# Kernel optimization log

Hardware: AMD Instinct MI355X
Metric: run time of the kernel (lower is better)

The kernel has to match this reference:

```python
import jax, jax.numpy as jnp
import numpy as np

H_DIM = 2048
D_FF = 4 * H_DIM
NUM_EXPERTS = 8
NUM_SHARED = 2
BATCH, SEQ = 2, 2048


def setup_inputs() -> dict:
    key = jax.random.key(0)
    ks = jax.random.split(key, 10)
    s = 0.02
    return {
        "x": jax.random.normal(ks[0], (BATCH, SEQ, H_DIM), dtype=jnp.float32),
        "ws_w1": jax.random.normal(ks[1], (NUM_SHARED, H_DIM, D_FF), dtype=jnp.float32) * s,
        "ws_b1": jnp.zeros((NUM_SHARED, D_FF), dtype=jnp.float32),
        "ws_w2": jax.random.normal(ks[2], (NUM_SHARED, D_FF, H_DIM), dtype=jnp.float32) * s,
        "ws_b2": jnp.zeros((NUM_SHARED, H_DIM), dtype=jnp.float32),
        "we_w1": jax.random.normal(ks[3], (NUM_EXPERTS, H_DIM, D_FF), dtype=jnp.float32) * s,
        "we_b1": jnp.zeros((NUM_EXPERTS, D_FF), dtype=jnp.float32),
        "we_w2": jax.random.normal(ks[4], (NUM_EXPERTS, D_FF, H_DIM), dtype=jnp.float32) * s,
        "we_b2": jnp.zeros((NUM_EXPERTS, H_DIM), dtype=jnp.float32),
        "wg": jax.random.normal(ks[5], (H_DIM, NUM_EXPERTS), dtype=jnp.float32) * s,
        "top_k": 2,
    }


def reference(x, ws_w1, ws_b1, ws_w2, ws_b2, we_w1, we_b1, we_w2, we_b2, wg, top_k):
    B, S, D = x.shape
    xt = x.reshape(-1, D)  # [T, D], T = B*S
    T = xt.shape[0]

    # ---- shared experts: sum over NUM_SHARED dense MLPs ----
    hs = jax.nn.relu(jnp.einsum('td,ndf->ntf', xt, ws_w1) + ws_b1[:, None, :])
    shared = jnp.einsum('ntf,nfd->td', hs, ws_w2) + ws_b2.sum(axis=0)  # [T, D]

    # ---- sparse top-k routed MoE ----
    logits = xt @ wg                       # [T, E] router logits
    probs = jax.nn.softmax(logits, axis=-1)
    topv, topi = jax.lax.top_k(probs, top_k)
    gates = jnp.zeros_like(probs).at[jnp.arange(T)[:, None], topi].set(topv)  # [T, E]

    moe = jnp.zeros_like(xt)
    for e in range(we_w1.shape[0]):  # small fixed expert count
        he = jax.nn.relu(xt @ we_w1[e] + we_b1[e])
        ye = he @ we_w2[e] + we_b2[e]
        moe = moe + gates[:, e:e + 1] * ye

    out = (shared + moe).reshape(B, S, D)
    return out, logits
```

## Files before the change

kernel.cpp:

```cpp
#include <hip/hip_runtime.h>

#define TOKENS 4096
#define HD 2048
#define FF 8192
#define NE 8
#define NS 2
#define YHALF 33554432

typedef __attribute__((ext_vector_type(8))) short bf16x8;
typedef __attribute__((ext_vector_type(4))) float f32x4;

__device__ __forceinline__ unsigned rnd_bf(unsigned u) {
  return u + 0x7fffu + ((u >> 16) & 1u);
}
__device__ __forceinline__ unsigned short f2bf(float f) {
  unsigned u = __builtin_bit_cast(unsigned, f);
  return (unsigned short)(rnd_bf(u) >> 16);
}

#define GLDS16(gp, lp)                                                         \
  __builtin_amdgcn_global_load_lds(                                            \
      (const __attribute__((address_space(1))) unsigned*)(const void*)(gp),    \
      (__attribute__((address_space(3))) unsigned*)(lp), 16, 0, 0)

__global__ void cast_x_kernel(const float* __restrict__ x, unsigned short* __restrict__ xb) {
  const size_t i = ((size_t)blockIdx.x * 256 + threadIdx.x) * 4;
  float4 v = *(const float4*)(x + i);
  ushort4 o;
  o.x = f2bf(v.x); o.y = f2bf(v.y); o.z = f2bf(v.z); o.w = f2bf(v.w);
  *(ushort4*)(xb + i) = o;
}

__global__ void router_kernel(const float* __restrict__ x, const float* __restrict__ wg,
                              float* __restrict__ logits_out, int* __restrict__ topi,
                              float* __restrict__ topv, int* __restrict__ counts) {
  const int wave = threadIdx.x >> 6, lane = threadIdx.x & 63;
  const int t = blockIdx.x * 4 + wave;
  const float* xr = x + (size_t)t * HD;
  float acc[8];
#pragma unroll
  for (int e = 0; e < 8; ++e) acc[e] = 0.f;
  for (int d = lane; d < HD; d += 64) {
    const float xv = xr[d];
    const float4 w0 = *(const float4*)(wg + (size_t)d * 8);
    const float4 w1 = *(const float4*)(wg + (size_t)d * 8 + 4);
    acc[0] += xv * w0.x; acc[1] += xv * w0.y; acc[2] += xv * w0.z; acc[3] += xv * w0.w;
    acc[4] += xv * w1.x; acc[5] += xv * w1.y; acc[6] += xv * w1.z; acc[7] += xv * w1.w;
  }
#pragma unroll
  for (int e = 0; e < 8; ++e) {
#pragma unroll
    for (int off = 32; off > 0; off >>= 1) acc[e] += __shfl_xor(acc[e], off);
  }
  if (lane == 0) {
    *(float4*)(logits_out + (size_t)t * 8)     = make_float4(acc[0], acc[1], acc[2], acc[3]);
    *(float4*)(logits_out + (size_t)t * 8 + 4) = make_float4(acc[4], acc[5], acc[6], acc[7]);
    float mx = acc[0];
#pragma unroll
    for (int e = 1; e < 8; ++e) mx = fmaxf(mx, acc[e]);
    float p[8], s = 0.f;
#pragma unroll
    for (int e = 0; e < 8; ++e) { p[e] = expf(acc[e] - mx); s += p[e]; }
    const float inv = 1.f / s;
    int i1 = 0;
#pragma unroll
    for (int e = 1; e < 8; ++e) if (acc[e] > acc[i1]) i1 = e;
    int i2 = (i1 == 0) ? 1 : 0;
#pragma unroll
    for (int e = 0; e < 8; ++e) if (e != i1 && acc[e] > acc[i2]) i2 = e;
    topi[2 * t]     = i1; topv[2 * t]     = p[i1] * inv;
    topi[2 * t + 1] = i2; topv[2 * t + 1] = p[i2] * inv;
    atomicAdd(&counts[i1], 1);
    atomicAdd(&counts[i2], 1);
  }
}

__global__ void offs_kernel(const int* __restrict__ counts, int* __restrict__ offs,
                            int* __restrict__ cursors) {
  if (threadIdx.x == 0) {
    int r = 0;
    for (int e = 0; e < NE; ++e) { offs[e] = r; cursors[e] = r; r += counts[e]; }
  }
}

__global__ void gather_kernel(const unsigned short* __restrict__ xb,
                              const int* __restrict__ topi, const float* __restrict__ topv,
                              int* __restrict__ cursors, unsigned short* __restrict__ xg,
                              int* __restrict__ row_token, float* __restrict__ row_gate,
                              int* __restrict__ row_of) {
  const int wave = threadIdx.x >> 6, lane = threadIdx.x & 63;
  const int t = blockIdx.x * 4 + wave;
  const uint4* src = (const uint4*)(xb + (size_t)t * HD);
#pragma unroll
  for (int j = 0; j < 2; ++j) {
    const int e = topi[2 * t + j];
    int pos = 0;
    if (lane == 0) {
      pos = atomicAdd(&cursors[e], 1);
      row_token[pos] = t;
      row_gate[pos] = topv[2 * t + j];
      row_of[2 * t + j] = pos;
    }
    pos = __shfl(pos, 0);
    uint4* dst = (uint4*)(xg + (size_t)pos * HD);
#pragma unroll
    for (int c = lane; c < 256; c += 64) dst[c] = src[c];
  }
}

template <int K, int N>
__global__ __launch_bounds__(256) void pack_wt(const float* __restrict__ we,
                                               const float* __restrict__ ws,
                                               unsigned short* __restrict__ dstw) {
  const int e = blockIdx.z;
  const float* src = (e < NE) ? (we + (size_t)e * K * N) : (ws + (size_t)(e - NE) * K * N);
  unsigned short* dst = dstw + (size_t)e * K * N;
  const int nt = blockIdx.x * 64;
  const int kt = blockIdx.y * 64;
  __shared__ unsigned short t[64][73];
  const int tid = threadIdx.x;
  const int rr = tid >> 4, cc = (tid & 15) * 4;
#pragma unroll
  for (int i = 0; i < 4; ++i) {
    const int k = rr + i * 16;
    float4 v = *(const float4*)(src + (size_t)(kt + k) * N + nt + cc);
    t[k][cc + 0] = f2bf(v.x);
    t[k][cc + 1] = f2bf(v.y);
    t[k][cc + 2] = f2bf(v.z);
    t[k][cc + 3] = f2bf(v.w);
  }
  __syncthreads();
  const int nr = tid >> 2, kc = (tid & 3) * 16;
  unsigned u[8];
#pragma unroll
  for (int j = 0; j < 8; ++j)
    u[j] = (unsigned)t[kc + 2 * j][nr] | ((unsigned)t[kc + 2 * j + 1][nr] << 16);
  unsigned short* dp = dst + (size_t)(nt + nr) * K + kt + kc;
  uint4 v0; v0.x = u[0]; v0.y = u[1]; v0.z = u[2]; v0.w = u[3];
  uint4 v1; v1.x = u[4]; v1.y = u[5]; v1.z = u[6]; v1.w = u[7];
  *(uint4*)dp = v0;
  *(uint4*)(dp + 8) = v1;
}

template <int MS>
__device__ __forceinline__ void rd_a(bf16x8 (&d)[8], const unsigned short* base,
                                     int wr, int fr, int fq, int swz) {
#pragma unroll
  for (int mi = 0; mi < 4; ++mi)
#pragma unroll
    for (int ks = 0; ks < 2; ++ks)
      d[mi * 2 + ks] = *(const bf16x8*)(base + (wr * 128 + MS * 64 + mi * 16 + fr) * 64 +
                                        (((ks * 4 + fq) ^ swz) << 3));
}
template <int NSUB>
__device__ __forceinline__ void rd_b(bf16x8 (&d)[4], const unsigned short* base,
                                     int wc, int fr, int fq, int swz) {
#pragma unroll
  for (int ni = 0; ni < 2; ++ni)
#pragma unroll
    for (int ks = 0; ks < 2; ++ks)
      d[ni * 2 + ks] = *(const bf16x8*)(base + (wc * 64 + NSUB * 32 + ni * 16 + fr) * 64 +
                                        (((ks * 4 + fq) ^ swz) << 3));
}
template <int MS, int NSUB>
__device__ __forceinline__ void mm16(f32x4 (&acc)[8][4], const bf16x8 (&a)[8],
                                     const bf16x8 (&b)[4]) {
  __builtin_amdgcn_s_setprio(1);
#pragma unroll
  for (int mi = 0; mi < 4; ++mi)
#pragma unroll
    for (int ni = 0; ni < 2; ++ni)
#pragma unroll
      for (int ks = 0; ks < 2; ++ks)
        acc[MS * 4 + mi][NSUB * 2 + ni] = __builtin_amdgcn_mfma_f32_16x16x32_bf16(
            a[mi * 2 + ks], b[ni * 2 + ks], acc[MS * 4 + mi][NSUB * 2 + ni], 0, 0, 0);
  __builtin_amdgcn_s_setprio(0);
}

template <int K>
__device__ __forceinline__ void kloop(
    const unsigned short* __restrict__ A, const unsigned short* __restrict__ Bt,
    unsigned short* smem, int m0, int n0, f32x4 (&acc)[8][4],
    int wr, int wc, int fr, int fq, int swz,
    int wrA, int wcB, int lr8, int lc8, int scol, int kt0, int nkt) {
#define SAK(s, kt, b)                                                          \
  { const int r0_ = wrA + (s) * 64 + lr8;                                      \
    const unsigned short* s_ = A + (size_t)(m0 + r0_) * K + (kt) * 64 + scol;  \
    unsigned short* d_ = smem + (b) * 32768 + r0_ * 64 + lc8 * 8;              \
    GLDS16(s_, d_); GLDS16(s_ + (size_t)8 * K, d_ + 8 * 64); }
#define SBK(s, kt, b)                                                          \
  { const int r0_ = wcB + (s) * 32 + lr8;                                      \
    const unsigned short* s_ = Bt + (size_t)(n0 + r0_) * K + (kt) * 64 + scol; \
    unsigned short* d_ = smem + (b) * 32768 + 16384 + r0_ * 64 + lc8 * 8;      \
    GLDS16(s_, d_); GLDS16(s_ + (size_t)8 * K, d_ + 8 * 64); }

  SAK(0, kt0, 0); SAK(1, kt0, 0); SBK(0, kt0, 0); SBK(1, kt0, 0);
  SAK(0, kt0 + 1, 1); SAK(1, kt0 + 1, 1); SBK(0, kt0 + 1, 1); SBK(1, kt0 + 1, 1);
  asm volatile("s_waitcnt vmcnt(8)" ::: "memory");
  __builtin_amdgcn_s_barrier();

  bf16x8 a0[8], a1[8], b0[4], b1[4];
  rd_a<0>(a0, smem, wr, fr, fq, swz);
  rd_b<0>(b0, smem + 16384, wc, fr, fq, swz);

  for (int t = 0; t < nkt; ++t) {
    const int cur = t & 1;
    const int tp2 = kt0 + ((t + 2 < nkt) ? t + 2 : t);
    const unsigned short* As_c = smem + cur * 32768;
    const unsigned short* Bs_c = As_c + 16384;
    const unsigned short* As_n = smem + (cur ^ 1) * 32768;
    const unsigned short* Bs_n = As_n + 16384;
    rd_b<1>(b1, Bs_c, wc, fr, fq, swz);
    mm16<0, 0>(acc, a0, b0);
    rd_a<1>(a1, As_c, wr, fr, fq, swz);
    mm16<0, 1>(acc, a0, b1);
    asm volatile("s_waitcnt lgkmcnt(0)" ::: "memory");
    __builtin_amdgcn_s_barrier();
    __builtin_amdgcn_sched_barrier(0);
    SAK(0, tp2, cur); SBK(0, tp2, cur);
    mm16<1, 0>(acc, a1, b0);
    asm volatile("s_waitcnt vmcnt(4)" ::: "memory");
    __builtin_amdgcn_s_barrier();
    __builtin_amdgcn_sched_barrier(0);
    rd_a<0>(a0, As_n, wr, fr, fq, swz);
    rd_b<0>(b0, Bs_n, wc, fr, fq, swz);
    SAK(1, tp2, cur); SBK(1, tp2, cur);
    mm16<1, 1>(acc, a1, b1);
  }
#undef SAK
#undef SBK
}

__global__ __launch_bounds__(512, 2) void g1k(
    const unsigned short* __restrict__ Ash, const unsigned short* __restrict__ Art,
    const unsigned short* __restrict__ wt1,
    const float* __restrict__ bE, const float* __restrict__ bS,
    unsigned short* __restrict__ hout,
    const int* __restrict__ counts, const int* __restrict__ offs,
    int do_pack, const float* __restrict__ we_w2, const float* __restrict__ ws_w2,
    unsigned short* __restrict__ wt2) {
  constexpr int K = HD;
  constexpr int NBX = FF / 256;
  constexpr int NWG = NBX * 16;
  extern __shared__ unsigned short smem[];

  const int e = blockIdx.z;
  int M;
  const unsigned short* A;
  const float* bias;
  int hbase;
  if (e < NE) {
    M = counts[e];
    A = Art + (size_t)offs[e] * K;
    bias = bE + (size_t)e * FF;
    hbase = offs[e];
  } else {
    M = TOKENS;
    A = Ash;
    bias = bS + (size_t)(e - NE) * FF;
    hbase = 2 * TOKENS + (e - NE) * TOKENS;
  }
  const unsigned short* Bt = wt1 + (size_t)e * HD * FF;

  int flat = blockIdx.x + NBX * blockIdx.y;
  flat = (flat & 7) * (NWG >> 3) + (flat >> 3);
  const int m0 = (flat & 15) * 256;
  const int n0 = (flat >> 4) * 256;
  const int tid = threadIdx.x;

  if (m0 >= M) {
    if (!do_pack) return;
    int total = 0, prefix = 0;
    for (int e2 = 0; e2 < NE; ++e2) {
      int mb = (counts[e2] + 255) >> 8; if (mb > 16) mb = 16;
      const int inv = 32 * (16 - mb);
      if (e2 < e) prefix += inv;
      total += inv;
    }
    int mb_e = (counts[e] + 255) >> 8; if (mb_e > 16) mb_e = 16;
    const int m_idx = flat & 15, n_idx = flat >> 4;
    const int rank = prefix + n_idx * (16 - mb_e) + (m_idx - mb_e);
    unsigned short* ps = smem;
    const int NT = 10 * 128 * 32;
    const int kk = tid >> 3, cc = (tid & 7) * 8;
    float4 r0a, r0b;
    int i = rank;
    if (i < NT) {
      const int e2 = i >> 12, rem = i & 4095, ktt = rem >> 5, ntt = rem & 31;
      const float* src = (e2 < NE) ? (we_w2 + (size_t)e2 * FF * HD)
                                   : (ws_w2 + (size_t)(e2 - NE) * FF * HD);
      const float* sp = src + (size_t)(ktt * 64 + kk) * HD + ntt * 64 + cc;
      r0a = *(const float4*)sp; r0b = *(const float4*)(sp + 4);
    }
    int it = 0;
    while (i < NT) {
      const int inext = i + total;
      float4 r1a, r1b;
      if (inext < NT) {
        const int e2 = inext >> 12, rem = inext & 4095, ktt = rem >> 5, ntt = rem & 31;
        const float* src = (e2 < NE) ? (we_w2 + (size_t)e2 * FF * HD)
                                     : (ws_w2 + (size_t)(e2 - NE) * FF * HD);
        const float* sp = src + (size_t)(ktt * 64 + kk) * HD + ntt * 64 + cc;
        r1a = *(const float4*)sp; r1b = *(const float4*)(sp + 4);
      }
      unsigned short* pb = ps + (it & 1) * (64 * 73);
      {
        unsigned short* tp = pb + kk * 73 + cc;
        tp[0] = f2bf(r0a.x); tp[1] = f2bf(r0a.y); tp[2] = f2bf(r0a.z); tp[3] = f2bf(r0a.w);
        tp[4] = f2bf(r0b.x); tp[5] = f2bf(r0b.y); tp[6] = f2bf(r0b.z); tp[7] = f2bf(r0b.w);
      }
      __syncthreads();
      {
        const int e2 = i >> 12, rem = i & 4095, ktt = rem >> 5, ntt = rem & 31;
        unsigned short* dst = wt2 + (size_t)e2 * HD * FF;
        const int nn = tid >> 3, kc = (tid & 7) * 8;
        unsigned u[4];
#pragma unroll
        for (int j = 0; j < 4; ++j)
          u[j] = (unsigned)pb[(kc + 2 * j) * 73 + nn] |
                 ((unsigned)pb[(kc + 2 * j + 1) * 73 + nn] << 16);
        uint4 v; v.x = u[0]; v.y = u[1]; v.z = u[2]; v.w = u[3];
        *(uint4*)(dst + (size_t)(ntt * 64 + nn) * FF + ktt * 64 + kc) = v;
      }
      r0a = r1a; r0b = r1b;
      i = inext; ++it;
    }
    return;
  }

  const int wid = tid >> 6, ln = tid & 63;
  const int wr = wid >> 2, wc = wid & 3;
  const int fr = ln & 15, fq = ln >> 4;
  const int swz = fr & 7;
  const int lr8 = ln >> 3;
  const int lc8 = ln & 7;
  const int scol = (lc8 ^ lr8) << 3;
  const int wrA = wr * 128 + wc * 16;
  const int wcB = wc * 64 + wr * 16;

  f32x4 acc[8][4];
#pragma unroll
  for (int i = 0; i < 8; ++i)
#pragma unroll
    for (int j = 0; j < 4; ++j) acc[i][j] = (f32x4){0.f, 0.f, 0.f, 0.f};

  kloop<K>(A, Bt, smem, m0, n0, acc, wr, wc, fr, fq, swz, wrA, wcB, lr8, lc8, scol,
           0, K / 64);

#pragma unroll
  for (int nn = 0; nn < 4; ++nn) {
#pragma unroll
    for (int mm = 0; mm < 8; ++mm) {
      const int col = n0 + wc * 64 + (nn >> 1) * 32 + (nn & 1) * 16 + fr;
      const float bb = bias[col];
#pragma unroll
      for (int j = 0; j < 4; ++j) {
        const int r = m0 + wr * 128 + (mm >> 2) * 64 + (mm & 3) * 16 + fq * 4 + j;
        if (r < M) {
          float v = acc[mm][nn][j] + bb;
          v = v > 0.f ? v : 0.f;
          hout[(size_t)(hbase + r) * FF + col] = f2bf(v);
        }
      }
    }
  }
}

__global__ __launch_bounds__(512, 2) void g2k(
    const unsigned short* __restrict__ hbuf, const unsigned short* __restrict__ wt2,
    const float* __restrict__ bE, const float* __restrict__ bS,
    float* __restrict__ ybuf,
    const int* __restrict__ counts, const int* __restrict__ offs) {
  constexpr int K = FF;
  constexpr int NBX = HD / 256;
  constexpr int NWG = NBX * 16;
  extern __shared__ unsigned short smem[];

  const int z = blockIdx.z;
  const int e = (z < 10) ? z : z - 10;
  const int half = (z < 10) ? 0 : 1;
  int M;
  const unsigned short* A;
  const float* bias;
  int hbase;
  if (e < NE) {
    M = counts[e];
    A = hbuf + (size_t)offs[e] * K;
    bias = bE + (size_t)e * HD;
    hbase = offs[e];
  } else {
    M = TOKENS;
    hbase = 2 * TOKENS + (e - NE) * TOKENS;
    A = hbuf + (size_t)hbase * K;
    bias = bS + (size_t)(e - NE) * HD;
  }
  const unsigned short* Bt = wt2 + (size_t)e * HD * FF;
  float* yout = ybuf + (size_t)half * YHALF;

  int flat = blockIdx.x + NBX * blockIdx.y;
  flat = (flat & 7) * (NWG >> 3) + (flat >> 3);
  const int m0 = (flat & 15) * 256;
  const int n0 = (flat >> 4) * 256;
  if (m0 >= M) return;

  const int tid = threadIdx.x;
  const int wid = tid >> 6, ln = tid & 63;
  const int wr = wid >> 2, wc = wid & 3;
  const int fr = ln & 15, fq = ln >> 4;
  const int swz = fr & 7;
  const int lr8 = ln >> 3;
  const int lc8 = ln & 7;
  const int scol = (lc8 ^ lr8) << 3;
  const int wrA = wr * 128 + wc * 16;
  const int wcB = wc * 64 + wr * 16;

  f32x4 acc[8][4];
#pragma unroll
  for (int i = 0; i < 8; ++i)
#pragma unroll
    for (int j = 0; j < 4; ++j) acc[i][j] = (f32x4){0.f, 0.f, 0.f, 0.f};

  kloop<K>(A, Bt, smem, m0, n0, acc, wr, wc, fr, fq, swz, wrA, wcB, lr8, lc8, scol,
           half * 64, 64);

#pragma unroll
  for (int nn = 0; nn < 4; ++nn) {
#pragma unroll
    for (int mm = 0; mm < 8; ++mm) {
      const int colw = wc * 64 + (nn >> 1) * 32 + (nn & 1) * 16 + fr;
      const float bb = (half == 0) ? bias[n0 + colw] : 0.f;
#pragma unroll
      for (int j = 0; j < 4; ++j) {
        const int r = m0 + wr * 128 + (mm >> 2) * 64 + (mm & 3) * 16 + fq * 4 + j;
        if (r < M)
          yout[(size_t)(hbase + r) * HD + n0 + colw] = acc[mm][nn][j] + bb;
      }
    }
  }
}

__global__ __launch_bounds__(256) void reduce_kernel(
    const float* __restrict__ ybuf, const int* __restrict__ row_of,
    const float* __restrict__ topv, float* __restrict__ out) {
  const int t = blockIdx.x;
  const int d = threadIdx.x * 8;
  const float g0 = topv[2 * t], g1 = topv[2 * t + 1];
  const size_t r0 = (size_t)row_of[2 * t] * HD + d;
  const size_t r1 = (size_t)row_of[2 * t + 1] * HD + d;
  const size_t rs0 = (size_t)(2 * TOKENS + t) * HD + d;
  const size_t rs1 = (size_t)(3 * TOKENS + t) * HD + d;
  float* o = out + (size_t)t * HD + d;
#pragma unroll
  for (int q = 0; q < 2; ++q) {
    float4 r = {0.f, 0.f, 0.f, 0.f};
#pragma unroll
    for (int h = 0; h < 2; ++h) {
      const float* yb = ybuf + (size_t)h * YHALF;
      const float4 a = *(const float4*)(yb + rs0 + q * 4);
      const float4 b = *(const float4*)(yb + rs1 + q * 4);
      const float4 c = *(const float4*)(yb + r0 + q * 4);
      const float4 ee = *(const float4*)(yb + r1 + q * 4);
      r.x += a.x + b.x + g0 * c.x + g1 * ee.x;
      r.y += a.y + b.y + g0 * c.y + g1 * ee.y;
      r.z += a.z + b.z + g0 * c.z + g1 * ee.z;
      r.w += a.w + b.w + g0 * c.w + g1 * ee.w;
    }
    *(float4*)(o + q * 4) = r;
  }
}

extern "C" void kernel_launch(void* const* d_in, const int* in_sizes, int n_in,
                              void* d_out, int out_size, void* d_ws, size_t ws_size,
                              hipStream_t stream) {
  const float* x     = (const float*)d_in[0];
  const float* ws_w1 = (const float*)d_in[1];
  const float* ws_b1 = (const float*)d_in[2];
  const float* ws_w2 = (const float*)d_in[3];
  const float* ws_b2 = (const float*)d_in[4];
  const float* we_w1 = (const float*)d_in[5];
  const float* we_b1 = (const float*)d_in[6];
  const float* we_w2 = (const float*)d_in[7];
  const float* we_b2 = (const float*)d_in[8];
  const float* wg    = (const float*)d_in[9];

  float* out = (float*)d_out;
  float* logits = out + (size_t)TOKENS * HD;

  hipFuncSetAttribute(reinterpret_cast<const void*>(g1k),
                      hipFuncAttributeMaxDynamicSharedMemorySize, 131072);
  hipFuncSetAttribute(reinterpret_cast<const void*>(g2k),
                      hipFuncAttributeMaxDynamicSharedMemorySize, 131072);

  char* ws = (char*)d_ws;
  unsigned short* wt1  = (unsigned short*)ws;
  unsigned short* wt2  = (unsigned short*)(ws + 335544320);
  unsigned short* xb   = (unsigned short*)(ws + 671088640);
  unsigned short* xg   = (unsigned short*)(ws + 687865856);
  unsigned short* hbuf = (unsigned short*)(ws + 721944576);
  char* ctrl = ws + 990380032;
  float* ybuf = (float*)ws;
  int*   row_token = (int*)(ctrl);
  float* row_gate  = (float*)(ctrl + 32768);
  int*   topi      = (int*)(ctrl + 65536);
  float* topv      = (float*)(ctrl + 98304);
  int*   counts    = (int*)(ctrl + 131072);
  int*   offs      = (int*)(ctrl + 131104);
  int*   cursors   = (int*)(ctrl + 131136);
  int*   row_of    = (int*)(ctrl + 131168);

  hipMemsetAsync(counts, 0, NE * sizeof(int), stream);
  cast_x_kernel<<<8192, 256, 0, stream>>>(x, xb);
  router_kernel<<<1024, 256, 0, stream>>>(x, wg, logits, topi, topv, counts);
  offs_kernel<<<1, 64, 0, stream>>>(counts, offs, cursors);
  gather_kernel<<<1024, 256, 0, stream>>>(xb, topi, topv, cursors, xg,
                                          row_token, row_gate, row_of);
  pack_wt<HD, FF><<<dim3(FF / 64, HD / 64, 10), 256, 0, stream>>>(we_w1, ws_w1, wt1);
  g1k<<<dim3(32, 16, 10), 512, 131072, stream>>>(
      xb, xg, wt1, we_b1, ws_b1, hbuf, counts, offs, 1, we_w2, ws_w2, wt2);
  g2k<<<dim3(8, 16, 20), 512, 131072, stream>>>(
      hbuf, wt2, we_b2, ws_b2, ybuf, counts, offs);
  reduce_kernel<<<TOKENS, 256, 0, stream>>>(ybuf, row_of, topv, out);

  (void)in_sizes; (void)n_in; (void)out_size; (void)ws_size;
}
```

Measured before the change: 1.867 ms.

## Merge shared-expert down-projections into one K-loop and fold x cast into router

The second GEMM no longer splits K into two halves written to separate output buffers. Each routed expert now runs its full K range in one block, and the two shared experts are concatenated along K into a single 256-step loop, so the reduce reads three rows instead of eight. The bf16 cast of x is also moved into the router kernel, removing one launch and one pass over x. The cost is less grid parallelism in g2k (9 z-slices instead of 20), and the merged shared block runs twice as long, which can leave a tail of underused units.

```diff
diff --git a/kernel.cpp b/kernel.cpp
--- a/kernel.cpp
+++ b/kernel.cpp
@@ -5,7 +5,6 @@
 #define FF 8192
 #define NE 8
 #define NS 2
-#define YHALF 33554432
 
 typedef __attribute__((ext_vector_type(8))) short bf16x8;
 typedef __attribute__((ext_vector_type(4))) float f32x4;
@@ -23,25 +22,20 @@
       (const __attribute__((address_space(1))) unsigned*)(const void*)(gp),    \
       (__attribute__((address_space(3))) unsigned*)(lp), 16, 0, 0)
 
-__global__ void cast_x_kernel(const float* __restrict__ x, unsigned short* __restrict__ xb) {
-  const size_t i = ((size_t)blockIdx.x * 256 + threadIdx.x) * 4;
-  float4 v = *(const float4*)(x + i);
-  ushort4 o;
-  o.x = f2bf(v.x); o.y = f2bf(v.y); o.z = f2bf(v.z); o.w = f2bf(v.w);
-  *(ushort4*)(xb + i) = o;
-}
-
 __global__ void router_kernel(const float* __restrict__ x, const float* __restrict__ wg,
                               float* __restrict__ logits_out, int* __restrict__ topi,
-                              float* __restrict__ topv, int* __restrict__ counts) {
+                              float* __restrict__ topv, int* __restrict__ counts,
+                              unsigned short* __restrict__ xb) {
   const int wave = threadIdx.x >> 6, lane = threadIdx.x & 63;
   const int t = blockIdx.x * 4 + wave;
   const float* xr = x + (size_t)t * HD;
+  unsigned short* xbr = xb + (size_t)t * HD;
   float acc[8];
 #pragma unroll
   for (int e = 0; e < 8; ++e) acc[e] = 0.f;
   for (int d = lane; d < HD; d += 64) {
     const float xv = xr[d];
+    xbr[d] = f2bf(xv);
     const float4 w0 = *(const float4*)(wg + (size_t)d * 8);
     const float4 w1 = *(const float4*)(wg + (size_t)d * 8 + 4);
     acc[0] += xv * w0.x; acc[1] += xv * w0.y; acc[2] += xv * w0.z; acc[3] += xv * w0.w;
@@ -179,23 +173,28 @@
 
 template <int K>
 __device__ __forceinline__ void kloop(
-    const unsigned short* __restrict__ A, const unsigned short* __restrict__ Bt,
-    unsigned short* smem, int m0, int n0, f32x4 (&acc)[8][4],
+    const unsigned short* __restrict__ A, const unsigned short* __restrict__ A2,
+    const unsigned short* __restrict__ Bt, const unsigned short* __restrict__ Bt2,
+    int ksw, unsigned short* smem, int m0, int n0, f32x4 (&acc)[8][4],
     int wr, int wc, int fr, int fq, int swz,
-    int wrA, int wcB, int lr8, int lc8, int scol, int kt0, int nkt) {
+    int wrA, int wcB, int lr8, int lc8, int scol, int nkt) {
 #define SAK(s, kt, b)                                                          \
-  { const int r0_ = wrA + (s) * 64 + lr8;                                      \
-    const unsigned short* s_ = A + (size_t)(m0 + r0_) * K + (kt) * 64 + scol;  \
+  { int kl_ = (kt); const unsigned short* ab_ = A;                             \
+    if (kl_ >= ksw) { ab_ = A2; kl_ -= ksw; }                                  \
+    const int r0_ = wrA + (s) * 64 + lr8;                                      \
+    const unsigned short* s_ = ab_ + (size_t)(m0 + r0_) * K + kl_ * 64 + scol; \
     unsigned short* d_ = smem + (b) * 32768 + r0_ * 64 + lc8 * 8;              \
     GLDS16(s_, d_); GLDS16(s_ + (size_t)8 * K, d_ + 8 * 64); }
 #define SBK(s, kt, b)                                                          \
-  { const int r0_ = wcB + (s) * 32 + lr8;                                      \
-    const unsigned short* s_ = Bt + (size_t)(n0 + r0_) * K + (kt) * 64 + scol; \
+  { int kl_ = (kt); const unsigned short* bb_ = Bt;                            \
+    if (kl_ >= ksw) { bb_ = Bt2; kl_ -= ksw; }                                 \
+    const int r0_ = wcB + (s) * 32 + lr8;                                      \
+    const unsigned short* s_ = bb_ + (size_t)(n0 + r0_) * K + kl_ * 64 + scol; \
     unsigned short* d_ = smem + (b) * 32768 + 16384 + r0_ * 64 + lc8 * 8;      \
     GLDS16(s_, d_); GLDS16(s_ + (size_t)8 * K, d_ + 8 * 64); }
 
-  SAK(0, kt0, 0); SAK(1, kt0, 0); SBK(0, kt0, 0); SBK(1, kt0, 0);
-  SAK(0, kt0 + 1, 1); SAK(1, kt0 + 1, 1); SBK(0, kt0 + 1, 1); SBK(1, kt0 + 1, 1);
+  SAK(0, 0, 0); SAK(1, 0, 0); SBK(0, 0, 0); SBK(1, 0, 0);
+  SAK(0, 1, 1); SAK(1, 1, 1); SBK(0, 1, 1); SBK(1, 1, 1);
   asm volatile("s_waitcnt vmcnt(8)" ::: "memory");
   __builtin_amdgcn_s_barrier();
 
@@ -205,7 +204,7 @@
 
   for (int t = 0; t < nkt; ++t) {
     const int cur = t & 1;
-    const int tp2 = kt0 + ((t + 2 < nkt) ? t + 2 : t);
+    const int tp2 = (t + 2 < nkt) ? t + 2 : t;
     const unsigned short* As_c = smem + cur * 32768;
     const unsigned short* Bs_c = As_c + 16384;
     const unsigned short* As_n = smem + (cur ^ 1) * 32768;
@@ -344,8 +343,8 @@
 #pragma unroll
     for (int j = 0; j < 4; ++j) acc[i][j] = (f32x4){0.f, 0.f, 0.f, 0.f};
 
-  kloop<K>(A, Bt, smem, m0, n0, acc, wr, wc, fr, fq, swz, wrA, wcB, lr8, lc8, scol,
-           0, K / 64);
+  kloop<K>(A, A, Bt, Bt, 1 << 30, smem, m0, n0, acc, wr, wc, fr, fq, swz,
+           wrA, wcB, lr8, lc8, scol, K / 64);
 
 #pragma unroll
   for (int nn = 0; nn < 4; ++nn) {
@@ -376,26 +375,28 @@
   constexpr int NWG = NBX * 16;
   extern __shared__ unsigned short smem[];
 
-  const int z = blockIdx.z;
-  const int e = (z < 10) ? z : z - 10;
-  const int half = (z < 10) ? 0 : 1;
-  int M;
-  const unsigned short* A;
-  const float* bias;
-  int hbase;
-  if (e < NE) {
+  const int e = blockIdx.z;
+  const bool merged = (e == NE);
+  int M, nkt, ksw, hbase;
+  const unsigned short *A, *A2, *B, *B2;
+  const float *bias, *bias2;
+  if (!merged) {
     M = counts[e];
-    A = hbuf + (size_t)offs[e] * K;
-    bias = bE + (size_t)e * HD;
+    A = hbuf + (size_t)offs[e] * K;  A2 = A;
+    B = wt2 + (size_t)e * HD * FF;   B2 = B;
+    bias = bE + (size_t)e * HD;      bias2 = nullptr;
     hbase = offs[e];
+    nkt = 128; ksw = 1 << 30;
   } else {
     M = TOKENS;
-    hbase = 2 * TOKENS + (e - NE) * TOKENS;
-    A = hbuf + (size_t)hbase * K;
-    bias = bS + (size_t)(e - NE) * HD;
-  }
-  const unsigned short* Bt = wt2 + (size_t)e * HD * FF;
-  float* yout = ybuf + (size_t)half * YHALF;
+    A  = hbuf + (size_t)(2 * TOKENS) * K;
+    A2 = hbuf + (size_t)(3 * TOKENS) * K;
+    B  = wt2 + (size_t)NE * HD * FF;
+    B2 = wt2 + (size_t)(NE + 1) * HD * FF;
+    bias = bS;  bias2 = bS + HD;
+    hbase = 2 * TOKENS;
+    nkt = 256; ksw = 128;
+  }
 
   int flat = blockIdx.x + NBX * blockIdx.y;
   flat = (flat & 7) * (NWG >> 3) + (flat >> 3);
@@ -420,20 +421,21 @@
 #pragma unroll
     for (int j = 0; j < 4; ++j) acc[i][j] = (f32x4){0.f, 0.f, 0.f, 0.f};
 
-  kloop<K>(A, Bt, smem, m0, n0, acc, wr, wc, fr, fq, swz, wrA, wcB, lr8, lc8, scol,
-           half * 64, 64);
+  kloop<K>(A, A2, B, B2, ksw, smem, m0, n0, acc, wr, wc, fr, fq, swz,
+           wrA, wcB, lr8, lc8, scol, nkt);
 
 #pragma unroll
   for (int nn = 0; nn < 4; ++nn) {
 #pragma unroll
     for (int mm = 0; mm < 8; ++mm) {
       const int colw = wc * 64 + (nn >> 1) * 32 + (nn & 1) * 16 + fr;
-      const float bb = (half == 0) ? bias[n0 + colw] : 0.f;
+      float bb = bias[n0 + colw];
+      if (merged) bb += bias2[n0 + colw];
 #pragma unroll
       for (int j = 0; j < 4; ++j) {
         const int r = m0 + wr * 128 + (mm >> 2) * 64 + (mm & 3) * 16 + fq * 4 + j;
         if (r < M)
-          yout[(size_t)(hbase + r) * HD + n0 + colw] = acc[mm][nn][j] + bb;
+          ybuf[(size_t)(hbase + r) * HD + n0 + colw] = acc[mm][nn][j] + bb;
       }
     }
   }
@@ -445,26 +447,20 @@
   const int t = blockIdx.x;
   const int d = threadIdx.x * 8;
   const float g0 = topv[2 * t], g1 = topv[2 * t + 1];
-  const size_t r0 = (size_t)row_of[2 * t] * HD + d;
-  const size_t r1 = (size_t)row_of[2 * t + 1] * HD + d;
-  const size_t rs0 = (size_t)(2 * TOKENS + t) * HD + d;
-  const size_t rs1 = (size_t)(3 * TOKENS + t) * HD + d;
+  const float* y0 = ybuf + (size_t)row_of[2 * t] * HD + d;
+  const float* y1 = ybuf + (size_t)row_of[2 * t + 1] * HD + d;
+  const float* s0 = ybuf + (size_t)(2 * TOKENS + t) * HD + d;
   float* o = out + (size_t)t * HD + d;
 #pragma unroll
   for (int q = 0; q < 2; ++q) {
-    float4 r = {0.f, 0.f, 0.f, 0.f};
-#pragma unroll
-    for (int h = 0; h < 2; ++h) {
-      const float* yb = ybuf + (size_t)h * YHALF;
-      const float4 a = *(const float4*)(yb + rs0 + q * 4);
-      const float4 b = *(const float4*)(yb + rs1 + q * 4);
-      const float4 c = *(const float4*)(yb + r0 + q * 4);
-      const float4 ee = *(const float4*)(yb + r1 + q * 4);
-      r.x += a.x + b.x + g0 * c.x + g1 * ee.x;
-      r.y += a.y + b.y + g0 * c.y + g1 * ee.y;
-      r.z += a.z + b.z + g0 * c.z + g1 * ee.z;
-      r.w += a.w + b.w + g0 * c.w + g1 * ee.w;
-    }
+    const float4 a = *(const float4*)(s0 + q * 4);
+    const float4 c = *(const float4*)(y0 + q * 4);
+    const float4 e = *(const float4*)(y1 + q * 4);
+    float4 r;
+    r.x = a.x + g0 * c.x + g1 * e.x;
+    r.y = a.y + g0 * c.y + g1 * e.y;
+    r.z = a.z + g0 * c.z + g1 * e.z;
+    r.w = a.w + g0 * c.w + g1 * e.w;
     *(float4*)(o + q * 4) = r;
   }
 }
@@ -509,15 +505,14 @@
   int*   row_of    = (int*)(ctrl + 131168);
 
   hipMemsetAsync(counts, 0, NE * sizeof(int), stream);
-  cast_x_kernel<<<8192, 256, 0, stream>>>(x, xb);
-  router_kernel<<<1024, 256, 0, stream>>>(x, wg, logits, topi, topv, counts);
+  router_kernel<<<1024, 256, 0, stream>>>(x, wg, logits, topi, topv, counts, xb);
   offs_kernel<<<1, 64, 0, stream>>>(counts, offs, cursors);
   gather_kernel<<<1024, 256, 0, stream>>>(xb, topi, topv, cursors, xg,
                                           row_token, row_gate, row_of);
   pack_wt<HD, FF><<<dim3(FF / 64, HD / 64, 10), 256, 0, stream>>>(we_w1, ws_w1, wt1);
   g1k<<<dim3(32, 16, 10), 512, 131072, stream>>>(
       xb, xg, wt1, we_b1, ws_b1, hbuf, counts, offs, 1, we_w2, ws_w2, wt2);
-  g2k<<<dim3(8, 16, 20), 512, 131072, stream>>>(
+  g2k<<<dim3(8, 16, 9), 512, 131072, stream>>>(
       hbuf, wt2, we_b2, ws_b2, ybuf, counts, offs);
   reduce_kernel<<<TOKENS, 256, 0, stream>>>(ybuf, row_of, topv, out);
 
```

Result: no change. 1.861 ms (-0.4%).
